# Optimization experiments

Hardware: AMD Instinct MI355X
Metric: run time of the kernel (lower is better)

## Reference

```python
import jax, jax.numpy as jnp
import numpy as np


def setup_inputs() -> dict:
    key = jax.random.key(0)
    kq, kk, kv = jax.random.split(key, 3)
    B, H, S, D = 2, 8, 4096, 64
    return {
        "query": jax.random.normal(kq, (B, H, S, D), dtype=jnp.float32),
        "key": jax.random.normal(kk, (B, H, S, D), dtype=jnp.float32),
        "value": jax.random.normal(kv, (B, H, S, D), dtype=jnp.float32),
    }


def reference(query, key, value):
    # NOTE: the torch source overwrites sqrt(d) with d, so the divisor is D, not sqrt(D).
    d = query.shape[-1]
    # score: [B, H, S_q, S_k]
    score = jnp.einsum("bhqd,bhkd->bhqk", query, key) / d
    relu = jax.nn.relu(score)  # no softmax / row normalization
    out = jnp.einsum("bhqk,bhkd->bhqd", relu, value)
    return out
```

## Files before the change

### kernel.cpp

```cpp
#include <hip/hip_runtime.h>
#include <hip/hip_bf16.h>
#include <stdint.h>


#define NH 16
#define SEQ 4096
#define DD 64
#define HE (SEQ*DD)
#define HB (HE*2)
#define Q16_OFF 0
#define K16_OFF (NH*HB)
#define V16_OFF (2*NH*HB)
#define WS_NEED (3*NH*HB)

typedef __attribute__((ext_vector_type(8)))  short    bf16x8;
typedef __attribute__((ext_vector_type(16))) float    f32x16;
typedef __attribute__((ext_vector_type(4)))  uint32_t u32x4;

__device__ inline uint32_t f2bf1(float f) {
  return (uint32_t)__builtin_bit_cast(unsigned short, __float2bfloat16(f));
}
__device__ inline uint32_t pack2bf(float a, float b) {
  return f2bf1(a) | (f2bf1(b) << 16);
}
__device__ inline uint32_t relu2(uint32_t w) {
  uint32_t r;
  asm("v_pk_max_f16 %0, %1, 0" : "=v"(r) : "v"(w));
  return r;
}

__global__ __launch_bounds__(256) void prepass_kernel(const float* __restrict__ Q,
                                                      const float* __restrict__ K,
                                                      const float* __restrict__ V,
                                                      char* __restrict__ ws) {
  __shared__ float vt[64*65];
  int bx = blockIdx.x, tid = threadIdx.x;
  if (bx < 2048) {
    size_t base = ((size_t)bx*256 + tid)*8;
    const float4* s = (const float4*)(Q + base);
    float4 a = s[0], b = s[1];
    const float sc = 1.0f/64.0f;
    u32x4 o;
    o.x = pack2bf(a.x*sc, a.y*sc);
    o.y = pack2bf(a.z*sc, a.w*sc);
    o.z = pack2bf(b.x*sc, b.y*sc);
    o.w = pack2bf(b.z*sc, b.w*sc);
    *(u32x4*)(ws + Q16_OFF + base*2) = o;
  } else if (bx < 3072) {
    int tile = bx - 2048;
    int head = tile >> 6, t = tile & 63;
    int r = tid >> 2, c0 = (tid & 3) * 16;
    const float4* s4 = (const float4*)(K + (size_t)head*HE + ((size_t)(t*64 + r))*64 + c0);
    float4 f0 = s4[0], f1 = s4[1], f2 = s4[2], f3 = s4[3];
    u32x4 c_lo, c_hi;
    c_lo.x = pack2bf(f0.x, f0.y); c_lo.y = pack2bf(f0.z, f0.w);
    c_lo.z = pack2bf(f1.x, f1.y); c_lo.w = pack2bf(f1.z, f1.w);
    c_hi.x = pack2bf(f2.x, f2.y); c_hi.y = pack2bf(f2.z, f2.w);
    c_hi.z = pack2bf(f3.x, f3.y); c_hi.w = pack2bf(f3.z, f3.w);
    char* tb = ws + K16_OFF + ((size_t)head*64 + t)*8192;
    int sw = (r & 7) << 4;
    *(u32x4*)(tb + r*128 + ((c0*2)      ^ sw)) = c_lo;
    *(u32x4*)(tb + r*128 + ((c0*2 + 16) ^ sw)) = c_hi;
  } else {
    int tile = bx - 3072;
    int head = tile >> 6, t = tile & 63;
    int k = tid >> 2, c0 = (tid & 3)*16;
    const float4* s4 = (const float4*)(V + (size_t)head*HE + ((size_t)(t*64 + k))*64 + c0);
    float4 f0 = s4[0], f1 = s4[1], f2 = s4[2], f3 = s4[3];
    float tmp[16] = {f0.x,f0.y,f0.z,f0.w, f1.x,f1.y,f1.z,f1.w,
                     f2.x,f2.y,f2.z,f2.w, f3.x,f3.y,f3.z,f3.w};
    #pragma unroll
    for (int j = 0; j < 16; ++j) vt[k*65 + c0 + j] = tmp[j];
    __syncthreads();
    int d = tid >> 2, k0 = (tid & 3)*16;
    float v2[16];
    #pragma unroll
    for (int j = 0; j < 16; ++j) v2[j] = vt[(k0 + j)*65 + d];
    u32x4 c_lo, c_hi;
    c_lo.x = pack2bf(v2[0],  v2[1]);  c_lo.y = pack2bf(v2[2],  v2[3]);
    c_lo.z = pack2bf(v2[4],  v2[5]);  c_lo.w = pack2bf(v2[6],  v2[7]);
    c_hi.x = pack2bf(v2[8],  v2[9]);  c_hi.y = pack2bf(v2[10], v2[11]);
    c_hi.z = pack2bf(v2[12], v2[13]); c_hi.w = pack2bf(v2[14], v2[15]);
    char* tb = ws + V16_OFF + ((size_t)head*64 + t)*8192;
    int sw = (d & 7) << 4;
    *(u32x4*)(tb + d*128 + ((k0*2)      ^ sw)) = c_lo;
    *(u32x4*)(tb + d*128 + ((k0*2 + 16) ^ sw)) = c_hi;
  }
}

__global__ __launch_bounds__(256, 2) void attn_kernel(const char* __restrict__ ws,
                                                      float* __restrict__ out) {
  __shared__ __align__(16) char lds[8*8192];
  int bx = blockIdx.x;
  int head = bx >> 5, qblk = bx & 31;
  int tid = threadIdx.x;
  int lane = tid & 63, w = tid >> 6;
  int l31 = lane & 31, h = lane >> 5;
  int g  = w >> 1;
  int mq = w & 1;

  const char* q16 = ws + Q16_OFF + (size_t)head*HB;
  const char* k16 = ws + K16_OFF + (size_t)head*HB;
  const char* v16 = ws + V16_OFF + (size_t)head*HB;
  int qrow0 = qblk*128 + mq*64;

  bf16x8 qf[2][4];
  #pragma unroll
  for (int m = 0; m < 2; ++m)
    #pragma unroll
    for (int t = 0; t < 4; ++t)
      qf[m][t] = *(const bf16x8*)(q16 + ((size_t)(qrow0 + m*32 + l31)*64 + t*16 + h*8)*2);

  f32x16 kZero;
  #pragma unroll
  for (int i = 0; i < 16; ++i) kZero[i] = 0.f;

  f32x16 o[2][2];
  #pragma unroll
  for (int m = 0; m < 2; ++m)
    #pragma unroll
    for (int nd = 0; nd < 2; ++nd)
      #pragma unroll
      for (int i = 0; i < 16; ++i) o[m][nd][i] = 0.f;

  char* ldsg = lds + g*4*8192;

  auto stage = [&](int cur, int kt) {
    const char* ktile = k16 + (size_t)(g*32 + kt)*8192;
    const char* vtile = v16 + (size_t)(g*32 + kt)*8192;
    char* lk = ldsg + (cur*2 + 0)*8192;
    char* lv = ldsg + (cur*2 + 1)*8192;
    #pragma unroll
    for (int c = 0; c < 4; ++c) {
      int off = (mq*4 + c)*1024;
      __builtin_amdgcn_global_load_lds(
          (const __attribute__((address_space(1))) void*)(ktile + off + lane*16),
          (__attribute__((address_space(3))) void*)(lk + off), 16, 0, 0);
      __builtin_amdgcn_global_load_lds(
          (const __attribute__((address_space(1))) void*)(vtile + off + lane*16),
          (__attribute__((address_space(3))) void*)(lv + off), 16, 0, 0);
    }
  };

  auto compute = [&](int cur) {
    const char* lk = ldsg + (cur*2 + 0)*8192;
    const char* lv = ldsg + (cur*2 + 1)*8192;
    f32x16 st[2][2];
    #pragma unroll
    for (int n = 0; n < 2; ++n) {
      bf16x8 kf[4];
      int row = n*32 + l31;
      int sw = (row & 7) << 4;
      #pragma unroll
      for (int t = 0; t < 4; ++t)
        kf[t] = *(const bf16x8*)(lk + row*128 + ((t*32 + h*16) ^ sw));
      __builtin_amdgcn_s_setprio(1);
      #pragma unroll
      for (int m = 0; m < 2; ++m) {
        f32x16 acc = __builtin_amdgcn_mfma_f32_32x32x16_bf16(kf[0], qf[m][0], kZero, 0, 0, 0);
        #pragma unroll
        for (int t = 1; t < 4; ++t)
          acc = __builtin_amdgcn_mfma_f32_32x32x16_bf16(kf[t], qf[m][t], acc, 0, 0, 0);
        st[m][n] = acc;
      }
      __builtin_amdgcn_s_setprio(0);
    }
    bf16x8 vf[2][4];
    #pragma unroll
    for (int nd = 0; nd < 2; ++nd) {
      int row = nd*32 + l31;
      int sw = (row & 7) << 4;
      #pragma unroll
      for (int ks = 0; ks < 4; ++ks)
        vf[nd][ks] = *(const bf16x8*)(lv + row*128 + ((ks*32 + h*16) ^ sw));
    }
    bf16x8 pa[2][4];
    #pragma unroll
    for (int m = 0; m < 2; ++m)
      #pragma unroll
      for (int n = 0; n < 2; ++n)
        #pragma unroll
        for (int kn = 0; kn < 2; ++kn) {
          uint32_t a0 = pack2bf(st[m][n][kn*8+0], st[m][n][kn*8+1]);
          uint32_t b0 = pack2bf(st[m][n][kn*8+2], st[m][n][kn*8+3]);
          uint32_t a2 = pack2bf(st[m][n][kn*8+4], st[m][n][kn*8+5]);
          uint32_t b2 = pack2bf(st[m][n][kn*8+6], st[m][n][kn*8+7]);
          asm("v_permlane32_swap_b32 %0, %1" : "+v"(a0), "+v"(a2));
          asm("v_permlane32_swap_b32 %0, %1" : "+v"(b0), "+v"(b2));
          union { uint32_t u[4]; bf16x8 v; } pk;
          pk.u[0] = relu2(a0);
          pk.u[1] = relu2(b0);
          pk.u[2] = relu2(a2);
          pk.u[3] = relu2(b2);
          pa[m][n*2 + kn] = pk.v;
        }
    __builtin_amdgcn_s_setprio(1);
    #pragma unroll
    for (int m = 0; m < 2; ++m)
      #pragma unroll
      for (int nd = 0; nd < 2; ++nd)
        #pragma unroll
        for (int ks = 0; ks < 4; ++ks)
          o[m][nd] = __builtin_amdgcn_mfma_f32_32x32x16_bf16(pa[m][ks], vf[nd][ks], o[m][nd], 0, 0, 0);
    __builtin_amdgcn_s_setprio(0);
  };

  stage(0, 0);
  stage(1, 1);
  #pragma unroll 1
  for (int kt = 0; kt < 30; ++kt) {
    int cur = kt & 1;
    asm volatile("s_waitcnt vmcnt(8)" ::: "memory");
    __builtin_amdgcn_s_barrier();
    __builtin_amdgcn_sched_barrier(0);
    compute(cur);
    __builtin_amdgcn_sched_barrier(0);
    __builtin_amdgcn_s_barrier();
    stage(cur, kt + 2);
  }
  asm volatile("s_waitcnt vmcnt(8)" ::: "memory");
  __builtin_amdgcn_s_barrier();
  __builtin_amdgcn_sched_barrier(0);
  compute(0);
  __builtin_amdgcn_sched_barrier(0);
  __builtin_amdgcn_s_barrier();
  asm volatile("s_waitcnt vmcnt(0)" ::: "memory");
  __builtin_amdgcn_s_barrier();
  __builtin_amdgcn_sched_barrier(0);
  compute(1);

  __syncthreads();
  float* red = (float*)lds;
  if (g == 1) {
    #pragma unroll
    for (int m = 0; m < 2; ++m)
      #pragma unroll
      for (int nd = 0; nd < 2; ++nd)
        #pragma unroll
        for (int r = 0; r < 16; ++r) {
          int ql = m*32 + (r & 3) + 8*(r >> 2) + 4*h;
          red[mq*4096 + ql*64 + nd*32 + l31] = o[m][nd][r];
        }
  }
  __syncthreads();
  if (g == 0) {
    float* outh = out + (size_t)head*HE;
    #pragma unroll
    for (int m = 0; m < 2; ++m)
      #pragma unroll
      for (int nd = 0; nd < 2; ++nd)
        #pragma unroll
        for (int r = 0; r < 16; ++r) {
          int ql = m*32 + (r & 3) + 8*(r >> 2) + 4*h;
          float v = o[m][nd][r] + red[mq*4096 + ql*64 + nd*32 + l31];
          outh[(size_t)(qrow0 + ql)*64 + nd*32 + l31] = v;
        }
  }
}

extern "C" void kernel_launch(void* const* d_in, const int* in_sizes, int n_in,
                              void* d_out, int out_size, void* d_ws, size_t ws_size,
                              hipStream_t stream) {
  if (n_in < 3 || ws_size < (size_t)WS_NEED) return;
  const float* Q = (const float*)d_in[0];
  const float* K = (const float*)d_in[1];
  const float* V = (const float*)d_in[2];
  float* out = (float*)d_out;
  char* ws = (char*)d_ws;
  hipLaunchKernelGGL(prepass_kernel, dim3(4096), dim3(256), 0, stream, Q, K, V, ws);
  hipLaunchKernelGGL(attn_kernel,    dim3(512),  dim3(256), 0, stream, ws, out);
}
```

Measured before the change: 86.16 us.

## Split query rows across eight waves with 32 rows per wave

Doubles the block to 512 threads so each wave handles 32 query rows instead of 64, halving accumulator and Q-fragment registers per wave and raising resident waves. Staging is redistributed across the 256 threads of each key-group with adjusted vmcnt waits, and the final cross-group reduction is reindexed. The trade-off is that each wave still reads full K/V tiles from LDS, so LDS read traffic per MFMA doubles.

```diff
diff --git a/kernel.cpp b/kernel.cpp
--- a/kernel.cpp
+++ b/kernel.cpp
@@ -88,64 +88,61 @@
   }
 }
 
-__global__ __launch_bounds__(256, 2) void attn_kernel(const char* __restrict__ ws,
+__global__ __launch_bounds__(512, 4) void attn_kernel(const char* __restrict__ ws,
                                                       float* __restrict__ out) {
-  __shared__ __align__(16) char lds[8*8192];
+  __shared__ __align__(16) char lds[2*2*16384];
   int bx = blockIdx.x;
   int head = bx >> 5, qblk = bx & 31;
   int tid = threadIdx.x;
   int lane = tid & 63, w = tid >> 6;
   int l31 = lane & 31, h = lane >> 5;
-  int g  = w >> 1;
-  int mq = w & 1;
+  int g  = w >> 2;
+  int wq = w & 3;
+  int t2 = tid & 255;
 
   const char* q16 = ws + Q16_OFF + (size_t)head*HB;
   const char* k16 = ws + K16_OFF + (size_t)head*HB;
   const char* v16 = ws + V16_OFF + (size_t)head*HB;
-  int qrow0 = qblk*128 + mq*64;
-
-  bf16x8 qf[2][4];
+  int qrow0 = qblk*128 + wq*32;
+
+  bf16x8 qf[4];
   #pragma unroll
-  for (int m = 0; m < 2; ++m)
-    #pragma unroll
-    for (int t = 0; t < 4; ++t)
-      qf[m][t] = *(const bf16x8*)(q16 + ((size_t)(qrow0 + m*32 + l31)*64 + t*16 + h*8)*2);
+  for (int t = 0; t < 4; ++t)
+    qf[t] = *(const bf16x8*)(q16 + ((size_t)(qrow0 + l31)*64 + t*16 + h*8)*2);
 
   f32x16 kZero;
   #pragma unroll
   for (int i = 0; i < 16; ++i) kZero[i] = 0.f;
 
-  f32x16 o[2][2];
+  f32x16 o[2];
   #pragma unroll
-  for (int m = 0; m < 2; ++m)
-    #pragma unroll
-    for (int nd = 0; nd < 2; ++nd)
-      #pragma unroll
-      for (int i = 0; i < 16; ++i) o[m][nd][i] = 0.f;
-
-  char* ldsg = lds + g*4*8192;
+  for (int nd = 0; nd < 2; ++nd)
+    #pragma unroll
+    for (int i = 0; i < 16; ++i) o[nd][i] = 0.f;
+
+  char* ldsg = lds + g*32768;
 
   auto stage = [&](int cur, int kt) {
     const char* ktile = k16 + (size_t)(g*32 + kt)*8192;
     const char* vtile = v16 + (size_t)(g*32 + kt)*8192;
-    char* lk = ldsg + (cur*2 + 0)*8192;
-    char* lv = ldsg + (cur*2 + 1)*8192;
-    #pragma unroll
-    for (int c = 0; c < 4; ++c) {
-      int off = (mq*4 + c)*1024;
+    char* lk = ldsg + cur*16384;
+    char* lv = lk + 8192;
+    #pragma unroll
+    for (int c = 0; c < 2; ++c) {
+      int off = c*4096 + t2*16;
       __builtin_amdgcn_global_load_lds(
-          (const __attribute__((address_space(1))) void*)(ktile + off + lane*16),
+          (const __attribute__((address_space(1))) void*)(ktile + off),
           (__attribute__((address_space(3))) void*)(lk + off), 16, 0, 0);
       __builtin_amdgcn_global_load_lds(
-          (const __attribute__((address_space(1))) void*)(vtile + off + lane*16),
+          (const __attribute__((address_space(1))) void*)(vtile + off),
           (__attribute__((address_space(3))) void*)(lv + off), 16, 0, 0);
     }
   };
 
   auto compute = [&](int cur) {
-    const char* lk = ldsg + (cur*2 + 0)*8192;
-    const char* lv = ldsg + (cur*2 + 1)*8192;
-    f32x16 st[2][2];
+    const char* lk = ldsg + cur*16384;
+    const char* lv = lk + 8192;
+    f32x16 st[2];
     #pragma unroll
     for (int n = 0; n < 2; ++n) {
       bf16x8 kf[4];
@@ -155,14 +152,11 @@
       for (int t = 0; t < 4; ++t)
         kf[t] = *(const bf16x8*)(lk + row*128 + ((t*32 + h*16) ^ sw));
       __builtin_amdgcn_s_setprio(1);
-      #pragma unroll
-      for (int m = 0; m < 2; ++m) {
-        f32x16 acc = __builtin_amdgcn_mfma_f32_32x32x16_bf16(kf[0], qf[m][0], kZero, 0, 0, 0);
-        #pragma unroll
-        for (int t = 1; t < 4; ++t)
-          acc = __builtin_amdgcn_mfma_f32_32x32x16_bf16(kf[t], qf[m][t], acc, 0, 0, 0);
-        st[m][n] = acc;
-      }
+      f32x16 acc = __builtin_amdgcn_mfma_f32_32x32x16_bf16(kf[0], qf[0], kZero, 0, 0, 0);
+      #pragma unroll
+      for (int t = 1; t < 4; ++t)
+        acc = __builtin_amdgcn_mfma_f32_32x32x16_bf16(kf[t], qf[t], acc, 0, 0, 0);
+      st[n] = acc;
       __builtin_amdgcn_s_setprio(0);
     }
     bf16x8 vf[2][4];
@@ -174,34 +168,30 @@
       for (int ks = 0; ks < 4; ++ks)
         vf[nd][ks] = *(const bf16x8*)(lv + row*128 + ((ks*32 + h*16) ^ sw));
     }
-    bf16x8 pa[2][4];
-    #pragma unroll
-    for (int m = 0; m < 2; ++m)
-      #pragma unroll
-      for (int n = 0; n < 2; ++n)
-        #pragma unroll
-        for (int kn = 0; kn < 2; ++kn) {
-          uint32_t a0 = pack2bf(st[m][n][kn*8+0], st[m][n][kn*8+1]);
-          uint32_t b0 = pack2bf(st[m][n][kn*8+2], st[m][n][kn*8+3]);
-          uint32_t a2 = pack2bf(st[m][n][kn*8+4], st[m][n][kn*8+5]);
-          uint32_t b2 = pack2bf(st[m][n][kn*8+6], st[m][n][kn*8+7]);
-          asm("v_permlane32_swap_b32 %0, %1" : "+v"(a0), "+v"(a2));
-          asm("v_permlane32_swap_b32 %0, %1" : "+v"(b0), "+v"(b2));
-          union { uint32_t u[4]; bf16x8 v; } pk;
-          pk.u[0] = relu2(a0);
-          pk.u[1] = relu2(b0);
-          pk.u[2] = relu2(a2);
-          pk.u[3] = relu2(b2);
-          pa[m][n*2 + kn] = pk.v;
-        }
+    bf16x8 pa[4];
+    #pragma unroll
+    for (int n = 0; n < 2; ++n)
+      #pragma unroll
+      for (int kn = 0; kn < 2; ++kn) {
+        uint32_t a0 = pack2bf(st[n][kn*8+0], st[n][kn*8+1]);
+        uint32_t b0 = pack2bf(st[n][kn*8+2], st[n][kn*8+3]);
+        uint32_t a2 = pack2bf(st[n][kn*8+4], st[n][kn*8+5]);
+        uint32_t b2 = pack2bf(st[n][kn*8+6], st[n][kn*8+7]);
+        asm("v_permlane32_swap_b32 %0, %1" : "+v"(a0), "+v"(a2));
+        asm("v_permlane32_swap_b32 %0, %1" : "+v"(b0), "+v"(b2));
+        union { uint32_t u[4]; bf16x8 v; } pk;
+        pk.u[0] = relu2(a0);
+        pk.u[1] = relu2(b0);
+        pk.u[2] = relu2(a2);
+        pk.u[3] = relu2(b2);
+        pa[n*2 + kn] = pk.v;
+      }
     __builtin_amdgcn_s_setprio(1);
     #pragma unroll
-    for (int m = 0; m < 2; ++m)
-      #pragma unroll
-      for (int nd = 0; nd < 2; ++nd)
-        #pragma unroll
-        for (int ks = 0; ks < 4; ++ks)
-          o[m][nd] = __builtin_amdgcn_mfma_f32_32x32x16_bf16(pa[m][ks], vf[nd][ks], o[m][nd], 0, 0, 0);
+    for (int nd = 0; nd < 2; ++nd)
+      #pragma unroll
+      for (int ks = 0; ks < 4; ++ks)
+        o[nd] = __builtin_amdgcn_mfma_f32_32x32x16_bf16(pa[ks], vf[nd][ks], o[nd], 0, 0, 0);
     __builtin_amdgcn_s_setprio(0);
   };
 
@@ -210,7 +200,7 @@
   #pragma unroll 1
   for (int kt = 0; kt < 30; ++kt) {
     int cur = kt & 1;
-    asm volatile("s_waitcnt vmcnt(8)" ::: "memory");
+    asm volatile("s_waitcnt vmcnt(4)" ::: "memory");
     __builtin_amdgcn_s_barrier();
     __builtin_amdgcn_sched_barrier(0);
     compute(cur);
@@ -218,7 +208,7 @@
     __builtin_amdgcn_s_barrier();
     stage(cur, kt + 2);
   }
-  asm volatile("s_waitcnt vmcnt(8)" ::: "memory");
+  asm volatile("s_waitcnt vmcnt(4)" ::: "memory");
   __builtin_amdgcn_s_barrier();
   __builtin_amdgcn_sched_barrier(0);
   compute(0);
@@ -233,28 +223,24 @@
   float* red = (float*)lds;
   if (g == 1) {
     #pragma unroll
-    for (int m = 0; m < 2; ++m)
-      #pragma unroll
-      for (int nd = 0; nd < 2; ++nd)
-        #pragma unroll
-        for (int r = 0; r < 16; ++r) {
-          int ql = m*32 + (r & 3) + 8*(r >> 2) + 4*h;
-          red[mq*4096 + ql*64 + nd*32 + l31] = o[m][nd][r];
-        }
+    for (int nd = 0; nd < 2; ++nd)
+      #pragma unroll
+      for (int r = 0; r < 16; ++r) {
+        int ql = wq*32 + (r & 3) + 8*(r >> 2) + 4*h;
+        red[ql*64 + nd*32 + l31] = o[nd][r];
+      }
   }
   __syncthreads();
   if (g == 0) {
     float* outh = out + (size_t)head*HE;
     #pragma unroll
-    for (int m = 0; m < 2; ++m)
-      #pragma unroll
-      for (int nd = 0; nd < 2; ++nd)
-        #pragma unroll
-        for (int r = 0; r < 16; ++r) {
-          int ql = m*32 + (r & 3) + 8*(r >> 2) + 4*h;
-          float v = o[m][nd][r] + red[mq*4096 + ql*64 + nd*32 + l31];
-          outh[(size_t)(qrow0 + ql)*64 + nd*32 + l31] = v;
-        }
+    for (int nd = 0; nd < 2; ++nd)
+      #pragma unroll
+      for (int r = 0; r < 16; ++r) {
+        int ql = wq*32 + (r & 3) + 8*(r >> 2) + 4*h;
+        float v = o[nd][r] + red[ql*64 + nd*32 + l31];
+        outh[(size_t)(qblk*128 + ql)*64 + nd*32 + l31] = v;
+      }
   }
 }
 
@@ -268,5 +254,5 @@
   float* out = (float*)d_out;
   char* ws = (char*)d_ws;
   hipLaunchKernelGGL(prepass_kernel, dim3(4096), dim3(256), 0, stream, Q, K, V, ws);
-  hipLaunchKernelGGL(attn_kernel,    dim3(512),  dim3(256), 0, stream, ws, out);
-}
+  hipLaunchKernelGGL(attn_kernel,    dim3(512),  dim3(512), 0, stream, ws, out);
+}
```

Result: no change. 87.59 us (+1.7%).
